# Kernel tuning notes

Measured on AMD Instinct MI355X. Metric: run time of the kernel, lower is better.

Reference implementation:

```python
import jax, jax.numpy as jnp
import numpy as np
import math

B, N, T, D, H, NOUT = 32, 20, 100, 4, 128, 16
E = N * (N - 1)
EPS = 1e-5

def _conv1d(x, w, b):
    # x: [M, Cin, L], w: [Cout, Cin, K] -> [M, Cout, L-K+1] (VALID, stride 1)
    y = jax.lax.conv_general_dilated(x, w, (1,), 'VALID', dimension_numbers=('NCH', 'OIH', 'NCH'))
    return y + b[None, :, None]

def _bn(x, g, b, axes, caxis):
    # training-mode batch norm (biased variance), eps as in torch
    m = jnp.mean(x, axis=axes, keepdims=True)
    v = jnp.var(x, axis=axes, keepdims=True)
    sh = [1] * x.ndim
    sh[caxis] = -1
    return (x - m) / jnp.sqrt(v + EPS) * g.reshape(sh) + b.reshape(sh)

def _mlp(x, w1, b1, w2, b2, g, bb):
    h = jax.nn.elu(x @ w1.T + b1)
    h = jax.nn.elu(h @ w2.T + b2)
    return _bn(h, g, bb, (0, 1), 2)  # BN over B*E samples per feature

def _forward(rel_rec, rel_send, inputs, conv1_w, conv1_b, bn1_g, bn1_b, conv2_w, conv2_b, bn2_g, bn2_b, pred_w, pred_b, att_w, att_b, mlp1_w1, mlp1_b1, mlp1_w2, mlp1_b2, mlp1_g, mlp1_bb, mlp2_w1, mlp2_b1, mlp2_w2, mlp2_b2, mlp2_g, mlp2_bb, mlp3_w1, mlp3_b1, mlp3_w2, mlp3_b2, mlp3_g, mlp3_bb, fc_out_w, fc_out_b):
    Bv, Nv, Tv, Dv = inputs.shape
    Ev = Nv * (Nv - 1)
    # node2edge_temporal: gather sender/receiver trajectories -> [B*E, 2D, T]
    xf = inputs.reshape(Bv, Nv, Tv * Dv)
    recv = jnp.einsum('en,bnf->bef', rel_rec, xf).reshape(Bv * Ev, Tv, Dv).transpose(0, 2, 1)
    send = jnp.einsum('en,bnf->bef', rel_send, xf).reshape(Bv * Ev, Tv, Dv).transpose(0, 2, 1)
    edges = jnp.concatenate([send, recv], axis=1)
    # CNN over time
    h = jax.nn.relu(_conv1d(edges, conv1_w, conv1_b))
    h = _bn(h, bn1_g, bn1_b, (0, 2), 1)
    L = h.shape[-1] // 2
    h = h[:, :, : 2 * L].reshape(h.shape[0], h.shape[1], L, 2).max(axis=-1)  # maxpool k=2 s=2
    h = jax.nn.relu(_conv1d(h, conv2_w, conv2_b))
    h = _bn(h, bn2_g, bn2_b, (0, 2), 1)
    pred = jnp.einsum('bct,oc->bot', h, pred_w[:, :, 0]) + pred_b[None, :, None]
    att = jax.nn.softmax(jnp.einsum('bct,oc->bot', h, att_w[:, :, 0]) + att_b[None, :, None], axis=-1)
    x = (pred * att).mean(axis=-1).reshape(Bv, Ev, -1)  # attention-weighted mean pool
    x = _mlp(x, mlp1_w1, mlp1_b1, mlp1_w2, mlp1_b2, mlp1_g, mlp1_bb)
    x_skip = x
    # edge2node: scatter-mean into receivers (divide by N)
    xn = jnp.einsum('en,beh->bnh', rel_rec, x) / Nv
    xn = _mlp(xn, mlp2_w1, mlp2_b1, mlp2_w2, mlp2_b2, mlp2_g, mlp2_bb)
    # node2edge: gather back to edges
    es = jnp.einsum('en,bnh->beh', rel_send, xn)
    er = jnp.einsum('en,bnh->beh', rel_rec, xn)
    x = jnp.concatenate([es, er, x_skip], axis=2)
    x = _mlp(x, mlp3_w1, mlp3_b1, mlp3_w2, mlp3_b2, mlp3_g, mlp3_bb)
    return x @ fc_out_w.T + fc_out_b

def setup_inputs() -> dict:
    key = jax.random.key(0)
    ks = iter(jax.random.split(key, 64))
    def rn(shape, scale):
        return jax.random.normal(next(ks), shape, dtype=jnp.float32) * scale
    def xav(fo, fi):
        return rn((fo, fi), math.sqrt(2.0 / (fo + fi)))
    inputs = rn((B, N, T, D), 1.0)
    pairs = np.array([(i, j) for i in range(N) for j in range(N) if i != j])
    eye = np.eye(N, dtype=np.float32)
    d = {'inputs': inputs,
         'rel_rec': jnp.asarray(eye[pairs[:, 0]]),
         'rel_send': jnp.asarray(eye[pairs[:, 1]])}
    d['conv1_w'] = rn((H, 2 * D, 5), math.sqrt(2.0 / (5 * H)))
    d['conv1_b'] = jnp.full((H,), 0.1, jnp.float32)
    d['bn1_g'] = jnp.ones((H,), jnp.float32); d['bn1_b'] = jnp.zeros((H,), jnp.float32)
    d['conv2_w'] = rn((H, H, 5), math.sqrt(2.0 / (5 * H)))
    d['conv2_b'] = jnp.full((H,), 0.1, jnp.float32)
    d['bn2_g'] = jnp.ones((H,), jnp.float32); d['bn2_b'] = jnp.zeros((H,), jnp.float32)
    d['pred_w'] = rn((H, H, 1), math.sqrt(2.0 / H))
    d['pred_b'] = jnp.full((H,), 0.1, jnp.float32)
    d['att_w'] = rn((1, H, 1), math.sqrt(2.0))
    d['att_b'] = jnp.full((1,), 0.1, jnp.float32)
    for nm, fi in (('mlp1', H), ('mlp2', H), ('mlp3', 3 * H)):
        d[nm + '_w1'] = xav(H, fi); d[nm + '_b1'] = jnp.full((H,), 0.1, jnp.float32)
        d[nm + '_w2'] = xav(H, H); d[nm + '_b2'] = jnp.full((H,), 0.1, jnp.float32)
        d[nm + '_g'] = jnp.ones((H,), jnp.float32); d[nm + '_bb'] = jnp.zeros((H,), jnp.float32)
    d['fc_out_w'] = xav(NOUT, H)
    d['fc_out_b'] = jnp.full((NOUT,), 0.1, jnp.float32)
    return d

def reference(inputs, rel_rec, rel_send, conv1_w, conv1_b, bn1_g, bn1_b, conv2_w, conv2_b, bn2_g, bn2_b, pred_w, pred_b, att_w, att_b, mlp1_w1, mlp1_b1, mlp1_w2, mlp1_b2, mlp1_g, mlp1_bb, mlp2_w1, mlp2_b1, mlp2_w2, mlp2_b2, mlp2_g, mlp2_bb, mlp3_w1, mlp3_b1, mlp3_w2, mlp3_b2, mlp3_g, mlp3_bb, fc_out_w, fc_out_b):
    return _forward(rel_rec, rel_send, inputs, conv1_w, conv1_b, bn1_g, bn1_b, conv2_w, conv2_b, bn2_g, bn2_b, pred_w, pred_b, att_w, att_b, mlp1_w1, mlp1_b1, mlp1_w2, mlp1_b2, mlp1_g, mlp1_bb, mlp2_w1, mlp2_b1, mlp2_w2, mlp2_b2, mlp2_g, mlp2_bb, mlp3_w1, mlp3_b1, mlp3_w2, mlp3_b2, mlp3_g, mlp3_bb, fc_out_w, fc_out_b)
```

## Files before the change

### kernel.cpp

```cpp
#include <hip/hip_runtime.h>
#include <hip/hip_bf16.h>
#include <hip/hip_fp16.h>

#define BB 32
#define NN 20
#define TT 100
#define DD 4
#define HH 128
#define EE 380
#define BE 12160
#define L1 96
#define LP 48
#define L2 44
#define NOUT 16
#define EPS 1e-5f
#define NREP 64

typedef _Float16 f16x8 __attribute__((ext_vector_type(8)));
typedef _Float16 f16x4 __attribute__((ext_vector_type(4)));
typedef _Float16 f16x2 __attribute__((ext_vector_type(2)));
typedef float f32x4 __attribute__((ext_vector_type(4)));

#define S_BIAS2 0
#define S_BN1_SC 256
#define S_BN2_SC 768

#define OFF_STATS 0ULL
#define OFF_SIDX 16384ULL
#define OFF_RIDX 18432ULL
#define OFF_INC 20480ULL
#define OFF_Y23 24576ULL
#define OFF_X 149446656ULL
#define OFF_BUFA 155672576ULL
#define OFF_BUFB 161898496ULL
#define OFF_XN 168124416ULL
#define OFF_T640 168452096ULL
#define OFF_REPM 168779776ULL
#define OFF_MP 171958272ULL
#define OFF_APACK OFF_T640
#define OFF_APACK1 (OFF_T640 + 163840ULL)
#define OFF_PWT (OFF_T640 + 180224ULL)
#define OFF_W2SUM (OFF_T640 + 245760ULL)
#define OFF_REP1 OFF_BUFA
#define OFF_REP2 (OFF_BUFA + 65536ULL)
#define MP_M1W1 0
#define MP_M1W2 16384
#define MP_M2W1 32768
#define MP_M2W2 49152
#define MP_M3W2 65536
#define MP_M3W1 81920

__device__ __forceinline__ float eluf(float v) { return v > 0.f ? v : expm1f(v); }

__global__ __launch_bounds__(256) void k_prep(const float* __restrict__ rel_rec,
                                              const float* __restrict__ rel_send,
                                              const float* __restrict__ w2,
                                              const float* __restrict__ w1,
                                              const float* __restrict__ pred_w,
                                              const float* __restrict__ m1w1,
                                              const float* __restrict__ m1w2,
                                              const float* __restrict__ m2w1,
                                              const float* __restrict__ m2w2,
                                              const float* __restrict__ m3w1,
                                              const float* __restrict__ m3w2,
                                              _Float16* __restrict__ apack,
                                              _Float16* __restrict__ apack1,
                                              float* __restrict__ pwt,
                                              float* __restrict__ w2sum,
                                              _Float16* __restrict__ mp,
                                              float* rep1, float* rep2, float* repm,
                                              int* sidx, int* ridx, int* inc) {
    int b = blockIdx.x;
    int tid = threadIdx.x;
    int l = tid & 63;
    if (b < 40) {
        int f = b * 4 + (tid >> 6);
        int m0 = f & 7, ks = f >> 3, s = ks & 3, k = ks >> 2;
        int m = m0 * 16 + (l & 15);
        int cbase = 32 * s + (l >> 4) * 8;
#pragma unroll
        for (int j = 0; j < 8; ++j)
            apack[(f * 64 + l) * 8 + j] = (_Float16)w2[m * 640 + (cbase + j) * 5 + k];
    } else if (b < 44) {
        int f = (b - 40) * 4 + (tid >> 6);
        int m0 = f & 7, s = f >> 3;
        int m = m0 * 16 + (l & 15);
        int cbase = 32 * s + (l >> 4) * 8;
#pragma unroll
        for (int j = 0; j < 8; ++j) {
            int c = cbase + j;
            int k = c >> 3, ci = c & 7;
            apack1[(f * 64 + l) * 8 + j] = (k < 5) ? (_Float16)w1[m * 40 + ci * 5 + k]
                                                   : (_Float16)0.f;
        }
    } else if (b == 44) {
        for (int i = tid; i < NREP * 256; i += 256) { rep1[i] = 0.f; rep2[i] = 0.f; }
        for (int i = tid; i < 3 * NREP * 256; i += 256) repm[i] = 0.f;
        for (int e = tid; e < EE; e += 256) {
            int s = 0, r = 0;
            for (int n = 0; n < NN; ++n) {
                if (rel_send[e * NN + n] > 0.5f) s = n;
                if (rel_rec[e * NN + n] > 0.5f) r = n;
            }
            sidx[e] = s; ridx[e] = r;
        }
        __syncthreads();
        if (tid < NN) {
            int k = 0;
            for (int e = 0; e < EE; ++e)
                if (ridx[e] == tid) inc[tid * (NN - 1) + (k++)] = e;
        }
    } else if (b < 53) {
        int idx = (b - 45) * 2048 + tid;
        for (int rep = 0; rep < 8; ++rep, idx += 256) {
            int o = idx >> 7, c = idx & 127;
            pwt[c * 128 + o] = pred_w[idx];
        }
    } else if (b < 117) {
        int idx = b - 53;
        const float* W; _Float16* dst; int K;
        if (idx < 8)       { W = m1w1; dst = mp + MP_M1W1; K = 128; }
        else if (idx < 16) { W = m1w2; dst = mp + MP_M1W2; K = 128; idx -= 8; }
        else if (idx < 24) { W = m2w1; dst = mp + MP_M2W1; K = 128; idx -= 16; }
        else if (idx < 32) { W = m2w2; dst = mp + MP_M2W2; K = 128; idx -= 24; }
        else if (idx < 40) { W = m3w2; dst = mp + MP_M3W2; K = 128; idx -= 32; }
        else               { W = m3w1; dst = mp + MP_M3W1; K = 384; idx -= 40; }
        int f = idx * 4 + (tid >> 6);
        int s = f >> 3, m0 = f & 7;
        int m = m0 * 16 + (l & 15);
        int cb = 32 * s + (l >> 4) * 8;
#pragma unroll
        for (int j = 0; j < 8; ++j)
            dst[(f * 64 + l) * 8 + j] = (_Float16)W[m * K + cb + j];
    } else {
        int idx = (b - 117) * 2048 + tid;
        for (int rep = 0; rep < 8; ++rep, idx += 256) {
            const float* wr = w2 + idx * 5;
            w2sum[idx] = wr[0] + wr[1] + wr[2] + wr[3] + wr[4];
        }
    }
}

__global__ __launch_bounds__(256) void k_conv1_stats(const float* __restrict__ inputs,
                                                     const _Float16* __restrict__ apack1,
                                                     const float* __restrict__ conv1_b,
                                                     const int* __restrict__ sidx,
                                                     const int* __restrict__ ridx,
                                                     float* rep1,
                                                     _Float16* __restrict__ y2p) {
    __shared__ __align__(16) _Float16 s_edgesT[104 * 8];
    __shared__ __align__(16) _Float16 s_y2t[48 * 136];
    int be = blockIdx.x;
    int b = be / EE, e = be - b * EE;
    int sn = sidx[e], rn = ridx[e];
    float* rep = rep1 + (be & (NREP - 1)) * 256;
    for (int i = threadIdx.x; i < 200; i += 256) {
        int side = (i >= 100) ? 1 : 0;
        int t = i - side * 100;
        int n = side ? rn : sn;
        float4 v = *(const float4*)(inputs + ((long long)(b * NN + n) * TT + t) * DD);
        f16x4 o = {(_Float16)v.x, (_Float16)v.y, (_Float16)v.z, (_Float16)v.w};
        *(f16x4*)(&s_edgesT[t * 8 + side * 4]) = o;
    }
    if (threadIdx.x < 32) s_edgesT[800 + threadIdx.x] = (_Float16)0.f;
    __syncthreads();
    int w = threadIdx.x >> 6, lane = threadIdx.x & 63;
    int quad = lane >> 4, l15 = lane & 15;
    f32x4 acc1[2][6];
#pragma unroll
    for (int m = 0; m < 2; ++m)
#pragma unroll
        for (int nt = 0; nt < 6; ++nt) acc1[m][nt] = (f32x4){0.f, 0.f, 0.f, 0.f};
    {
        const f16x8* Ap = (const f16x8*)apack1;
#pragma unroll
        for (int s = 0; s < 2; ++s) {
            f16x8 a0 = Ap[(s * 8 + 2 * w) * 64 + lane];
            f16x8 a1 = Ap[(s * 8 + 2 * w + 1) * 64 + lane];
#pragma unroll
            for (int nt = 0; nt < 6; ++nt) {
                f16x8 bfr = *(const f16x8*)(&s_edgesT[(nt * 16 + l15 + 4 * s + quad) * 8]);
                acc1[0][nt] = __builtin_amdgcn_mfma_f32_16x16x32_f16(a0, bfr, acc1[0][nt], 0, 0, 0);
                acc1[1][nt] = __builtin_amdgcn_mfma_f32_16x16x32_f16(a1, bfr, acc1[1][nt], 0, 0, 0);
            }
        }
    }
#pragma unroll
    for (int m = 0; m < 2; ++m) {
        int co0 = (2 * w + m) * 16 + quad * 4;
        float ss[4] = {0.f, 0.f, 0.f, 0.f}, qq[4] = {0.f, 0.f, 0.f, 0.f};
#pragma unroll
        for (int nt = 0; nt < 6; ++nt) {
            int t = nt * 16 + l15;
#pragma unroll
            for (int r = 0; r < 4; ++r) {
                float v = fmaxf(acc1[m][nt][r] + conv1_b[co0 + r], 0.f);
                ss[r] += v; qq[r] += v * v;
                float p = __shfl_xor(v, 1);
                if ((l15 & 1) == 0)
                    s_y2t[(t >> 1) * 136 + co0 + r] = (_Float16)fmaxf(v, p);
            }
        }
#pragma unroll
        for (int r = 0; r < 4; ++r) {
            float s = ss[r], q = qq[r];
            s += __shfl_xor(s, 1); s += __shfl_xor(s, 2); s += __shfl_xor(s, 4); s += __shfl_xor(s, 8);
            q += __shfl_xor(q, 1); q += __shfl_xor(q, 2); q += __shfl_xor(q, 4); q += __shfl_xor(q, 8);
            if (l15 == 0) {
                atomicAdd(&rep[co0 + r], s);
                atomicAdd(&rep[128 + co0 + r], q);
            }
        }
    }
    __syncthreads();
    _Float16* dst = y2p + (long long)be * 6144;
    for (int chunk = threadIdx.x; chunk < 768; chunk += 256) {
        int row = chunk >> 4, off = (chunk & 15) * 8;
        *(f16x8*)(dst + row * 128 + off) = *(const f16x8*)(&s_y2t[row * 136 + off]);
    }
}

__global__ void k_finalize_rep(float* __restrict__ rep, float* stats, int scIdx,
                               const float* __restrict__ g, const float* __restrict__ bb,
                               float inv_count) {
    int j = threadIdx.x;
    float s = 0.f, q = 0.f;
    for (int i = 0; i < NREP; ++i) {
        s += rep[i * 256 + j];
        q += rep[i * 256 + 128 + j];
    }
    for (int i = 0; i < NREP; ++i) {
        rep[i * 256 + j] = 0.f;
        rep[i * 256 + 128 + j] = 0.f;
    }
    float m = s * inv_count;
    float v = fmaxf(q * inv_count - m * m, 0.f);
    float sc = g[j] * rsqrtf(v + EPS);
    stats[scIdx + j] = sc;
    stats[scIdx + 128 + j] = bb[j] - m * sc;
}

__global__ void k_finalize_bn1(float* __restrict__ rep, float* stats,
                               const float* __restrict__ g, const float* __restrict__ bb,
                               const float* __restrict__ w2sum, const float* __restrict__ conv2_b,
                               float inv_count) {
    __shared__ float s_sh[128];
    int j = threadIdx.x;
    float s = 0.f, q = 0.f;
    for (int i = 0; i < NREP; ++i) {
        s += rep[i * 256 + j];
        q += rep[i * 256 + 128 + j];
    }
    for (int i = 0; i < NREP; ++i) {
        rep[i * 256 + j] = 0.f;
        rep[i * 256 + 128 + j] = 0.f;
    }
    float m = s * inv_count;
    float v = fmaxf(q * inv_count - m * m, 0.f);
    float sc = g[j] * rsqrtf(v + EPS);
    float sh = bb[j] - m * sc;
    stats[S_BN1_SC + j] = sc;
    stats[S_BN1_SC + 128 + j] = sh;
    s_sh[j] = sh;
    __syncthreads();
    float acc = conv2_b[j];
    for (int ci = 0; ci < 128; ++ci)
        acc = fmaf(w2sum[j * 128 + ci], s_sh[ci], acc);
    stats[S_BIAS2 + j] = acc;
}

__global__ __launch_bounds__(256) void k_scale(_Float16* __restrict__ apack,
                                               const float* __restrict__ stats) {
    int tid = threadIdx.x, l = tid & 63;
    int f = blockIdx.x * 4 + (tid >> 6);
    int s = (f >> 3) & 3;
    int cbase = 32 * s + (l >> 4) * 8;
    _Float16* p = apack + (f * 64 + l) * 8;
#pragma unroll
    for (int j = 0; j < 8; ++j)
        p[j] = (_Float16)((float)p[j] * stats[S_BN1_SC + cbase + j]);
}

__global__ __launch_bounds__(512, 6) void k_conv2(_Float16* __restrict__ y23,
                                                  const _Float16* __restrict__ apack,
                                                  const float* __restrict__ stats,
                                                  float* rep2) {
    __shared__ __align__(16) _Float16 s_y2t[2][48 * 136];
    int tid = threadIdx.x;
    long long be0 = (long long)blockIdx.x * 2;
    for (int i = tid; i < 1536; i += 512) {
        int ed = i / 768, rem = i - ed * 768;
        *(f16x8*)(&s_y2t[ed][(rem >> 4) * 136 + (rem & 15) * 8]) =
            *(const f16x8*)(y23 + (be0 + ed) * 6144 + rem * 8);
    }
    __syncthreads();
    int w = tid >> 6, lane = tid & 63;
    int quad = lane >> 4, l15 = lane & 15;
    int g2 = w & 3, ep = w >> 2;
    const char* base = (const char*)&s_y2t[ep][0];
    int rb0 = quad * 16 + l15 * 272;
    f32x4 acc[2][3];
#pragma unroll
    for (int m = 0; m < 2; ++m)
#pragma unroll
        for (int nt = 0; nt < 3; ++nt) acc[m][nt] = (f32x4){0.f, 0.f, 0.f, 0.f};
    const f16x8* Ap = (const f16x8*)apack;
    f16x8 amA[2], amB[2];
#pragma unroll
    for (int m = 0; m < 2; ++m) amA[m] = Ap[(g2 * 2 + m) * 64 + lane];
#define C2_STEP(AM, IT)                                                               \
    do {                                                                              \
        int k = (IT) >> 2, s = (IT) & 3;                                              \
        int rbase = k * 272 + s * 64 + rb0;                                           \
        _Pragma("unroll")                                                             \
        for (int nt = 0; nt < 3; ++nt) {                                              \
            int ro = rbase + nt * (16 * 272);                                         \
            if (nt == 2) { int rr = 32 + l15 + k; if (rr > 47) ro -= (rr - 47) * 272; } \
            f16x8 bfr = *(const f16x8*)(base + ro);                                   \
            acc[0][nt] = __builtin_amdgcn_mfma_f32_16x16x32_f16(AM[0], bfr, acc[0][nt], 0, 0, 0); \
            acc[1][nt] = __builtin_amdgcn_mfma_f32_16x16x32_f16(AM[1], bfr, acc[1][nt], 0, 0, 0); \
        }                                                                             \
    } while (0)
    for (int it = 0; it < 20; it += 2) {
#pragma unroll
        for (int m = 0; m < 2; ++m) amB[m] = Ap[((it + 1) * 8 + g2 * 2 + m) * 64 + lane];
        C2_STEP(amA, it);
        if (it + 2 < 20) {
#pragma unroll
            for (int m = 0; m < 2; ++m) amA[m] = Ap[((it + 2) * 8 + g2 * 2 + m) * 64 + lane];
        }
        C2_STEP(amB, it + 1);
    }
#undef C2_STEP
    long long be = be0 + ep;
    _Float16* y3 = y23 + be * 6144;
    float* rep = rep2 + ((int)(be & (NREP - 1))) * 256;
#pragma unroll
    for (int m = 0; m < 2; ++m) {
        int co0 = (g2 * 2 + m) * 16 + quad * 4;
        float4 bs = *(const float4*)(stats + S_BIAS2 + co0);
        float ssum[4] = {0.f, 0.f, 0.f, 0.f}, qsum[4] = {0.f, 0.f, 0.f, 0.f};
#pragma unroll
        for (int nt = 0; nt < 3; ++nt) {
            int t = nt * 16 + l15;
            if (t < 44) {
                float v0 = fmaxf(acc[m][nt][0] + bs.x, 0.f);
                float v1 = fmaxf(acc[m][nt][1] + bs.y, 0.f);
                float v2 = fmaxf(acc[m][nt][2] + bs.z, 0.f);
                float v3 = fmaxf(acc[m][nt][3] + bs.w, 0.f);
                f16x4 o = {(_Float16)v0, (_Float16)v1, (_Float16)v2, (_Float16)v3};
                *(f16x4*)(y3 + t * 128 + co0) = o;
                ssum[0] += v0; qsum[0] += v0 * v0;
                ssum[1] += v1; qsum[1] += v1 * v1;
                ssum[2] += v2; qsum[2] += v2 * v2;
                ssum[3] += v3; qsum[3] += v3 * v3;
            }
        }
#pragma unroll
        for (int r = 0; r < 4; ++r) {
            float s = ssum[r], q = qsum[r];
            s += __shfl_xor(s, 1); s += __shfl_xor(s, 2); s += __shfl_xor(s, 4); s += __shfl_xor(s, 8);
            q += __shfl_xor(q, 1); q += __shfl_xor(q, 2); q += __shfl_xor(q, 4); q += __shfl_xor(q, 8);
            if (l15 == 0) {
                atomicAdd(&rep[co0 + r], s);
                atomicAdd(&rep[128 + co0 + r], q);
            }
        }
    }
}

__global__ __launch_bounds__(256) void k_predatt(const _Float16* __restrict__ y23,
                                                 const float* __restrict__ stats,
                                                 const float* __restrict__ att_w,
                                                 const float* __restrict__ att_b,
                                                 const float* __restrict__ pwt,
                                                 const float* __restrict__ pred_b,
                                                 float* __restrict__ x) {
    __shared__ float h[44 * 132];
    __shared__ float s_att[48];
    __shared__ float s_p1[256];
    __shared__ float s_p2[256];
    __shared__ float s_sc[128], s_sh[128];
    int be = blockIdx.x, tid = threadIdx.x;
    if (tid < 128) {
        s_sc[tid] = stats[S_BN2_SC + tid];
        s_sh[tid] = stats[S_BN2_SC + 128 + tid];
    }
    __syncthreads();
    const _Float16* yp = y23 + (long long)be * 6144;
    for (int i = tid; i < 704; i += 256) {
        int t = i >> 4, c0 = (i & 15) * 8;
        f16x8 v = *(const f16x8*)(yp + i * 8);
        float4 a, bq;
        a.x = fmaf((float)v[0], s_sc[c0 + 0], s_sh[c0 + 0]);
        a.y = fmaf((float)v[1], s_sc[c0 + 1], s_sh[c0 + 1]);
        a.z = fmaf((float)v[2], s_sc[c0 + 2], s_sh[c0 + 2]);
        a.w = fmaf((float)v[3], s_sc[c0 + 3], s_sh[c0 + 3]);
        bq.x = fmaf((float)v[4], s_sc[c0 + 4], s_sh[c0 + 4]);
        bq.y = fmaf((float)v[5], s_sc[c0 + 5], s_sh[c0 + 5]);
        bq.z = fmaf((float)v[6], s_sc[c0 + 6], s_sh[c0 + 6]);
        bq.w = fmaf((float)v[7], s_sc[c0 + 7], s_sh[c0 + 7]);
        *(float4*)(&h[t * 132 + c0]) = a;
        *(float4*)(&h[t * 132 + c0 + 4]) = bq;
    }
    __syncthreads();
    int w = tid >> 6, lane = tid & 63;
    {
        float aw0 = att_w[lane], aw1 = att_w[64 + lane];
        for (int tt = 0; tt < 11; ++tt) {
            int t = w * 11 + tt;
            float p = h[t * 132 + lane] * aw0 + h[t * 132 + 64 + lane] * aw1;
            p += __shfl_xor(p, 1); p += __shfl_xor(p, 2); p += __shfl_xor(p, 4);
            p += __shfl_xor(p, 8); p += __shfl_xor(p, 16); p += __shfl_xor(p, 32);
            if (lane == 0) s_att[t] = p + att_b[0];
        }
    }
    __syncthreads();
    if (w == 0) {
        float v = (lane < 44) ? s_att[lane] : -1e30f;
        float m = v;
        m = fmaxf(m, __shfl_xor(m, 1)); m = fmaxf(m, __shfl_xor(m, 2));
        m = fmaxf(m, __shfl_xor(m, 4)); m = fmaxf(m, __shfl_xor(m, 8));
        m = fmaxf(m, __shfl_xor(m, 16)); m = fmaxf(m, __shfl_xor(m, 32));
        float ev = (lane < 44) ? expf(v - m) : 0.f;
        float ss = ev;
        ss += __shfl_xor(ss, 1); ss += __shfl_xor(ss, 2); ss += __shfl_xor(ss, 4);
        ss += __shfl_xor(ss, 8); ss += __shfl_xor(ss, 16); ss += __shfl_xor(ss, 32);
        if (lane < 44) s_att[lane] = ev / ss;
    }
    __syncthreads();
    {
        int c = tid & 127, hh = tid >> 7;
        float a = 0.f;
        for (int t = hh * 22; t < hh * 22 + 22; ++t) a = fmaf(h[t * 132 + c], s_att[t], a);
        s_p1[tid] = a;
    }
    __syncthreads();
    {
        int o = tid & 127, hh = tid >> 7;
        float a = 0.f;
        for (int c = hh * 64; c < hh * 64 + 64; ++c) {
            float hw = s_p1[c] + s_p1[128 + c];
            a = fmaf(pwt[c * 128 + o], hw, a);
        }
        s_p2[tid] = a;
    }
    __syncthreads();
    if (tid < 128) {
        float a = s_p2[tid] + s_p2[128 + tid] + pred_b[tid];
        x[(long long)be * 128 + tid] = a * (1.0f / 44.0f);
    }
}

__global__ __launch_bounds__(256) void k_mlp2x(const float* __restrict__ in,
                                               const _Float16* __restrict__ wp1,
                                               const float* __restrict__ b1,
                                               const _Float16* __restrict__ wp2,
                                               const float* __restrict__ b2,
                                               float* __restrict__ out,
                                               float* __restrict__ repm) {
    __shared__ __align__(16) _Float16 s_in[64 * 136];
    __shared__ __align__(16) _Float16 s_mid[64 * 136];
    int tid = threadIdx.x;
    long long r0 = (long long)blockIdx.x * 64;
    {
        const float4* src = (const float4*)(in + r0 * 128);
        for (int i = tid; i < 2048; i += 256) {
            int row = i >> 5, c0 = (i & 31) * 4;
            float4 v = src[i];
            f16x4 o = {(_Float16)v.x, (_Float16)v.y, (_Float16)v.z, (_Float16)v.w};
            *(f16x4*)(&s_in[row * 136 + c0]) = o;
        }
    }
    __syncthreads();
    int w = tid >> 6, lane = tid & 63, quad = lane >> 4, l15 = lane & 15;
    {
        f32x4 acc[2][4];
#pragma unroll
        for (int m = 0; m < 2; ++m)
#pragma unroll
            for (int nt = 0; nt < 4; ++nt) acc[m][nt] = (f32x4){0.f, 0.f, 0.f, 0.f};
        const f16x8* Ap = (const f16x8*)wp1;
#pragma unroll
        for (int s = 0; s < 4; ++s) {
            f16x8 a0 = Ap[(s * 8 + 2 * w) * 64 + lane];
            f16x8 a1 = Ap[(s * 8 + 2 * w + 1) * 64 + lane];
#pragma unroll
            for (int nt = 0; nt < 4; ++nt) {
                f16x8 bfr = *(const f16x8*)((const char*)s_in + (nt * 16 + l15) * 272 + 64 * s + quad * 16);
                acc[0][nt] = __builtin_amdgcn_mfma_f32_16x16x32_f16(a0, bfr, acc[0][nt], 0, 0, 0);
                acc[1][nt] = __builtin_amdgcn_mfma_f32_16x16x32_f16(a1, bfr, acc[1][nt], 0, 0, 0);
            }
        }
#pragma unroll
        for (int m = 0; m < 2; ++m) {
            int j0 = (2 * w + m) * 16 + quad * 4;
            float4 bs = *(const float4*)(b1 + j0);
#pragma unroll
            for (int nt = 0; nt < 4; ++nt) {
                int row = nt * 16 + l15;
                f16x4 o = {(_Float16)eluf(acc[m][nt][0] + bs.x),
                           (_Float16)eluf(acc[m][nt][1] + bs.y),
                           (_Float16)eluf(acc[m][nt][2] + bs.z),
                           (_Float16)eluf(acc[m][nt][3] + bs.w)};
                *(f16x4*)(&s_mid[row * 136 + j0]) = o;
            }
        }
    }
    __syncthreads();
    {
        f32x4 acc[2][4];
#pragma unroll
        for (int m = 0; m < 2; ++m)
#pragma unroll
            for (int nt = 0; nt < 4; ++nt) acc[m][nt] = (f32x4){0.f, 0.f, 0.f, 0.f};
        const f16x8* Ap = (const f16x8*)wp2;
#pragma unroll
        for (int s = 0; s < 4; ++s) {
            f16x8 a0 = Ap[(s * 8 + 2 * w) * 64 + lane];
            f16x8 a1 = Ap[(s * 8 + 2 * w + 1) * 64 + lane];
#pragma unroll
            for (int nt = 0; nt < 4; ++nt) {
                f16x8 bfr = *(const f16x8*)((const char*)s_mid + (nt * 16 + l15) * 272 + 64 * s + quad * 16);
                acc[0][nt] = __builtin_amdgcn_mfma_f32_16x16x32_f16(a0, bfr, acc[0][nt], 0, 0, 0);
                acc[1][nt] = __builtin_amdgcn_mfma_f32_16x16x32_f16(a1, bfr, acc[1][nt], 0, 0, 0);
            }
        }
#pragma unroll
        for (int m = 0; m < 2; ++m) {
            int j0 = (2 * w + m) * 16 + quad * 4;
            float4 bs = *(const float4*)(b2 + j0);
            float ss[4] = {0.f, 0.f, 0.f, 0.f}, qq[4] = {0.f, 0.f, 0.f, 0.f};
#pragma unroll
            for (int nt = 0; nt < 4; ++nt) {
                int row = nt * 16 + l15;
                float v0 = eluf(acc[m][nt][0] + bs.x);
                float v1 = eluf(acc[m][nt][1] + bs.y);
                float v2 = eluf(acc[m][nt][2] + bs.z);
                float v3 = eluf(acc[m][nt][3] + bs.w);
                float4 o = {v0, v1, v2, v3};
                *(float4*)(out + (r0 + row) * 128 + j0) = o;
                ss[0] += v0; qq[0] += v0 * v0;
                ss[1] += v1; qq[1] += v1 * v1;
                ss[2] += v2; qq[2] += v2 * v2;
                ss[3] += v3; qq[3] += v3 * v3;
            }
            float* rep = repm + (blockIdx.x & (NREP - 1)) * 256;
#pragma unroll
            for (int r = 0; r < 4; ++r) {
                float s = ss[r], q = qq[r];
                s += __shfl_xor(s, 1); s += __shfl_xor(s, 2); s += __shfl_xor(s, 4); s += __shfl_xor(s, 8);
                q += __shfl_xor(q, 1); q += __shfl_xor(q, 2); q += __shfl_xor(q, 4); q += __shfl_xor(q, 8);
                if (l15 == 0) {
                    atomicAdd(&rep[j0 + r], s);
                    atomicAdd(&rep[128 + j0 + r], q);
                }
            }
        }
    }
}

__global__ __launch_bounds__(256) void k_mlp3x(const float* __restrict__ xn,
                                               const float* __restrict__ bufB,
                                               const int* __restrict__ sidx,
                                               const int* __restrict__ ridx,
                                               const float* __restrict__ repm1,
                                               const float* __restrict__ repm2,
                                               const float* __restrict__ m1g,
                                               const float* __restrict__ m1bb,
                                               const float* __restrict__ m2g,
                                               const float* __restrict__ m2bb,
                                               const _Float16* __restrict__ wp1,
                                               const float* __restrict__ b1,
                                               const _Float16* __restrict__ wp2,
                                               const float* __restrict__ b2,
                                               float* __restrict__ out,
                                               float* __restrict__ repm3) {
    __shared__ __align__(16) _Float16 s_b[64 * 392];
    __shared__ __align__(16) _Float16 s_mid[64 * 136];
    __shared__ float s_st[4][128];
    __shared__ int s_s[64], s_r[64];
    int tid = threadIdx.x;
    long long r0 = (long long)blockIdx.x * 64;
    if (tid < 128) {
        float s = 0.f, q = 0.f;
        for (int i = 0; i < NREP; ++i) {
            s += repm2[i * 256 + tid];
            q += repm2[i * 256 + 128 + tid];
        }
        float mm = s * (1.0f / (float)(BB * NN));
        float vv = fmaxf(q * (1.0f / (float)(BB * NN)) - mm * mm, 0.f);
        float sc = m2g[tid] * rsqrtf(vv + EPS);
        s_st[0][tid] = sc;
        s_st[1][tid] = m2bb[tid] - mm * sc;
        s = 0.f; q = 0.f;
        for (int i = 0; i < NREP; ++i) {
            s += repm1[i * 256 + tid];
            q += repm1[i * 256 + 128 + tid];
        }
        mm = s * (1.0f / (float)BE);
        vv = fmaxf(q * (1.0f / (float)BE) - mm * mm, 0.f);
        sc = m1g[tid] * rsqrtf(vv + EPS);
        s_st[2][tid] = sc;
        s_st[3][tid] = m1bb[tid] - mm * sc;
    }
    if (tid < 64) {
        int r = (int)r0 + tid, b = r / EE, ed = r - b * EE;
        s_s[tid] = (b * NN + sidx[ed]) * 128;
        s_r[tid] = (b * NN + ridx[ed]) * 128;
    }
    __syncthreads();
    for (int i = tid; i < 8192; i += 256) {
        int row = i >> 7, j = i & 127;
        float sc2 = s_st[0][j], sh2 = s_st[1][j];
        s_b[row * 392 + j] = (_Float16)fmaf(xn[s_s[row] + j], sc2, sh2);
        s_b[row * 392 + 128 + j] = (_Float16)fmaf(xn[s_r[row] + j], sc2, sh2);
        s_b[row * 392 + 256 + j] = (_Float16)fmaf(bufB[(r0 + row) * 128 + j], s_st[2][j], s_st[3][j]);
    }
    __syncthreads();
    int w = tid >> 6, lane = tid & 63, quad = lane >> 4, l15 = lane & 15;
    {
        f32x4 acc[2][4];
#pragma unroll
        for (int m = 0; m < 2; ++m)
#pragma unroll
            for (int nt = 0; nt < 4; ++nt) acc[m][nt] = (f32x4){0.f, 0.f, 0.f, 0.f};
        const f16x8* Ap = (const f16x8*)wp1;
#pragma unroll
        for (int s = 0; s < 12; ++s) {
            f16x8 a0 = Ap[(s * 8 + 2 * w) * 64 + lane];
            f16x8 a1 = Ap[(s * 8 + 2 * w + 1) * 64 + lane];
#pragma unroll
            for (int nt = 0; nt < 4; ++nt) {
                f16x8 bfr = *(const f16x8*)((const char*)s_b + (nt * 16 + l15) * 784 + 64 * s + quad * 16);
                acc[0][nt] = __builtin_amdgcn_mfma_f32_16x16x32_f16(a0, bfr, acc[0][nt], 0, 0, 0);
                acc[1][nt] = __builtin_amdgcn_mfma_f32_16x16x32_f16(a1, bfr, acc[1][nt], 0, 0, 0);
            }
        }
#pragma unroll
        for (int m = 0; m < 2; ++m) {
            int j0 = (2 * w + m) * 16 + quad * 4;
            float4 bs = *(const float4*)(b1 + j0);
#pragma unroll
            for (int nt = 0; nt < 4; ++nt) {
                int row = nt * 16 + l15;
                f16x4 o = {(_Float16)eluf(acc[m][nt][0] + bs.x),
                           (_Float16)eluf(acc[m][nt][1] + bs.y),
                           (_Float16)eluf(acc[m][nt][2] + bs.z),
                           (_Float16)eluf(acc[m][nt][3] + bs.w)};
                *(f16x4*)(&s_mid[row * 136 + j0]) = o;
            }
        }
    }
    __syncthreads();
    {
        f32x4 acc[2][4];
#pragma unroll
        for (int m = 0; m < 2; ++m)
#pragma unroll
            for (int nt = 0; nt < 4; ++nt) acc[m][nt] = (f32x4){0.f, 0.f, 0.f, 0.f};
        const f16x8* Ap = (const f16x8*)wp2;
#pragma unroll
        for (int s = 0; s < 4; ++s) {
            f16x8 a0 = Ap[(s * 8 + 2 * w) * 64 + lane];
            f16x8 a1 = Ap[(s * 8 + 2 * w + 1) * 64 + lane];
#pragma unroll
            for (int nt = 0; nt < 4; ++nt) {
                f16x8 bfr = *(const f16x8*)((const char*)s_mid + (nt * 16 + l15) * 272 + 64 * s + quad * 16);
                acc[0][nt] = __builtin_amdgcn_mfma_f32_16x16x32_f16(a0, bfr, acc[0][nt], 0, 0, 0);
                acc[1][nt] = __builtin_amdgcn_mfma_f32_16x16x32_f16(a1, bfr, acc[1][nt], 0, 0, 0);
            }
        }
#pragma unroll
        for (int m = 0; m < 2; ++m) {
            int j0 = (2 * w + m) * 16 + quad * 4;
            float4 bs = *(const float4*)(b2 + j0);
            float ss[4] = {0.f, 0.f, 0.f, 0.f}, qq[4] = {0.f, 0.f, 0.f, 0.f};
#pragma unroll
            for (int nt = 0; nt < 4; ++nt) {
                int row = nt * 16 + l15;
                float v0 = eluf(acc[m][nt][0] + bs.x);
                float v1 = eluf(acc[m][nt][1] + bs.y);
                float v2 = eluf(acc[m][nt][2] + bs.z);
                float v3 = eluf(acc[m][nt][3] + bs.w);
                float4 o = {v0, v1, v2, v3};
                *(float4*)(out + (r0 + row) * 128 + j0) = o;
                ss[0] += v0; qq[0] += v0 * v0;
                ss[1] += v1; qq[1] += v1 * v1;
                ss[2] += v2; qq[2] += v2 * v2;
                ss[3] += v3; qq[3] += v3 * v3;
            }
            float* rep = repm3 + (blockIdx.x & (NREP - 1)) * 256;
#pragma unroll
            for (int r = 0; r < 4; ++r) {
                float s = ss[r], q = qq[r];
                s += __shfl_xor(s, 1); s += __shfl_xor(s, 2); s += __shfl_xor(s, 4); s += __shfl_xor(s, 8);
                q += __shfl_xor(q, 1); q += __shfl_xor(q, 2); q += __shfl_xor(q, 4); q += __shfl_xor(q, 8);
                if (l15 == 0) {
                    atomicAdd(&rep[j0 + r], s);
                    atomicAdd(&rep[128 + j0 + r], q);
                }
            }
        }
    }
}

__global__ __launch_bounds__(128) void k_e2n(const float* __restrict__ bufB,
                                             const int* __restrict__ inc,
                                             const float* __restrict__ repm1,
                                             const float* __restrict__ m1g,
                                             const float* __restrict__ m1bb,
                                             float* __restrict__ xn) {
    int bn = blockIdx.x;
    int b = bn / NN, n = bn - b * NN;
    int j = threadIdx.x;
    float s0 = 0.f, q0 = 0.f;
    for (int i = 0; i < NREP; ++i) {
        s0 += repm1[i * 256 + j];
        q0 += repm1[i * 256 + 128 + j];
    }
    float mm = s0 * (1.0f / (float)BE);
    float vv = fmaxf(q0 * (1.0f / (float)BE) - mm * mm, 0.f);
    float sc = m1g[j] * rsqrtf(vv + EPS);
    float sh = m1bb[j] - mm * sc;
    float s = 0.f;
    for (int k = 0; k < NN - 1; ++k) {
        int e = inc[n * (NN - 1) + k];
        s += bufB[(long long)(b * EE + e) * 128 + j];
    }
    xn[bn * 128 + j] = (s * sc + (float)(NN - 1) * sh) * (1.0f / (float)NN);
}

__global__ __launch_bounds__(256) void k_fcout(const float* __restrict__ h2,
                                               const float* __restrict__ repm3,
                                               const float* __restrict__ m3g,
                                               const float* __restrict__ m3bb,
                                               const float* __restrict__ fcw,
                                               const float* __restrict__ fcb,
                                               float* __restrict__ out) {
    __shared__ float s_x[16 * 129];
    __shared__ float s_w[16 * 129];
    __shared__ float s_sc[128], s_sh[128];
    int r0 = blockIdx.x * 16;
    int tid = threadIdx.x;
    if (tid < 128) {
        float s = 0.f, q = 0.f;
        for (int i = 0; i < NREP; ++i) {
            s += repm3[i * 256 + tid];
            q += repm3[i * 256 + 128 + tid];
        }
        float mm = s * (1.0f / (float)BE);
        float vv = fmaxf(q * (1.0f / (float)BE) - mm * mm, 0.f);
        float sc = m3g[tid] * rsqrtf(vv + EPS);
        s_sc[tid] = sc;
        s_sh[tid] = m3bb[tid] - mm * sc;
    }
    __syncthreads();
    for (int i = tid; i < 16 * 128; i += 256) {
        int rr = i >> 7, j = i & 127;
        s_x[rr * 129 + j] = fmaf(h2[(long long)(r0 + rr) * 128 + j], s_sc[j], s_sh[j]);
    }
    for (int i = tid; i < 16 * 128; i += 256) {
        int o = i >> 7, j = i & 127;
        s_w[o * 129 + j] = fcw[i];
    }
    __syncthreads();
    int rl = tid >> 4, o = tid & 15;
    float a = fcb[o];
    for (int j = 0; j < 128; ++j) a = fmaf(s_x[rl * 129 + j], s_w[o * 129 + j], a);
    out[(long long)(r0 + rl) * 16 + o] = a;
}

extern "C" void kernel_launch(void* const* d_in, const int* in_sizes, int n_in,
                              void* d_out, int out_size, void* d_ws, size_t ws_size,
                              hipStream_t stream) {
    const float* inputs = (const float*)d_in[0];
    const float* rel_rec = (const float*)d_in[1];
    const float* rel_send = (const float*)d_in[2];
    const float* conv1_w = (const float*)d_in[3];
    const float* conv1_b = (const float*)d_in[4];
    const float* bn1_g = (const float*)d_in[5];
    const float* bn1_b = (const float*)d_in[6];
    const float* conv2_w = (const float*)d_in[7];
    const float* conv2_b = (const float*)d_in[8];
    const float* bn2_g = (const float*)d_in[9];
    const float* bn2_b = (const float*)d_in[10];
    const float* pred_w = (const float*)d_in[11];
    const float* pred_b = (const float*)d_in[12];
    const float* att_w = (const float*)d_in[13];
    const float* att_b = (const float*)d_in[14];
    const float* m1w1 = (const float*)d_in[15];
    const float* m1b1 = (const float*)d_in[16];
    const float* m1w2 = (const float*)d_in[17];
    const float* m1b2 = (const float*)d_in[18];
    const float* m1g = (const float*)d_in[19];
    const float* m1bb = (const float*)d_in[20];
    const float* m2w1 = (const float*)d_in[21];
    const float* m2b1 = (const float*)d_in[22];
    const float* m2w2 = (const float*)d_in[23];
    const float* m2b2 = (const float*)d_in[24];
    const float* m2g = (const float*)d_in[25];
    const float* m2bb = (const float*)d_in[26];
    const float* m3w1 = (const float*)d_in[27];
    const float* m3b1 = (const float*)d_in[28];
    const float* m3w2 = (const float*)d_in[29];
    const float* m3b2 = (const float*)d_in[30];
    const float* m3g = (const float*)d_in[31];
    const float* m3bb = (const float*)d_in[32];
    const float* fcw = (const float*)d_in[33];
    const float* fcb = (const float*)d_in[34];

    char* ws = (char*)d_ws;
    float* stats = (float*)(ws + OFF_STATS);
    int* sidx = (int*)(ws + OFF_SIDX);
    int* ridx = (int*)(ws + OFF_RIDX);
    int* inc = (int*)(ws + OFF_INC);
    _Float16* y23 = (_Float16*)(ws + OFF_Y23);
    float* x = (float*)(ws + OFF_X);
    float* bufB = (float*)(ws + OFF_BUFB);
    float* xn = (float*)(ws + OFF_XN);
    _Float16* apack = (_Float16*)(ws + OFF_APACK);
    _Float16* apack1 = (_Float16*)(ws + OFF_APACK1);
    float* pwt = (float*)(ws + OFF_PWT);
    float* w2sum = (float*)(ws + OFF_W2SUM);
    float* rep1 = (float*)(ws + OFF_REP1);
    float* rep2 = (float*)(ws + OFF_REP2);
    float* repm1 = (float*)(ws + OFF_REPM);
    float* repm2 = (float*)(ws + OFF_REPM + 65536ULL);
    float* repm3 = (float*)(ws + OFF_REPM + 131072ULL);
    _Float16* mp = (_Float16*)(ws + OFF_MP);
    float* outp = (float*)d_out;

    hipLaunchKernelGGL(k_prep, dim3(125), dim3(256), 0, stream,
                       rel_rec, rel_send, conv2_w, conv1_w, pred_w,
                       m1w1, m1w2, m2w1, m2w2, m3w1, m3w2,
                       apack, apack1, pwt, w2sum, mp, rep1, rep2, repm1, sidx, ridx, inc);
    hipLaunchKernelGGL(k_conv1_stats, dim3(BE), dim3(256), 0, stream,
                       inputs, apack1, conv1_b, sidx, ridx, rep1, y23);
    hipLaunchKernelGGL(k_finalize_bn1, dim3(1), dim3(128), 0, stream,
                       rep1, stats, bn1_g, bn1_b, w2sum, conv2_b, 1.0f / (float)(BE * L1));
    hipLaunchKernelGGL(k_scale, dim3(40), dim3(256), 0, stream, apack, stats);
    hipLaunchKernelGGL(k_conv2, dim3(BE / 2), dim3(512), 0, stream,
                       y23, apack, stats, rep2);
    hipLaunchKernelGGL(k_finalize_rep, dim3(1), dim3(128), 0, stream,
                       rep2, stats, S_BN2_SC, bn2_g, bn2_b, 1.0f / (float)(BE * L2));
    hipLaunchKernelGGL(k_predatt, dim3(BE), dim3(256), 0, stream,
                       y23, stats, att_w, att_b, pwt, pred_b, x);
    hipLaunchKernelGGL(k_mlp2x, dim3(BE / 64), dim3(256), 0, stream,
                       x, mp + MP_M1W1, m1b1, mp + MP_M1W2, m1b2, bufB, repm1);
    hipLaunchKernelGGL(k_e2n, dim3(BB * NN), dim3(128), 0, stream, bufB, inc, repm1, m1g, m1bb, xn);
    hipLaunchKernelGGL(k_mlp2x, dim3(BB * NN / 64), dim3(256), 0, stream,
                       xn, mp + MP_M2W1, m2b1, mp + MP_M2W2, m2b2, xn, repm2);
    hipLaunchKernelGGL(k_mlp3x, dim3(BE / 64), dim3(256), 0, stream,
                       xn, bufB, sidx, ridx, repm1, repm2, m1g, m1bb, m2g, m2bb,
                       mp + MP_M3W1, m3b1, mp + MP_M3W2, m3b2, bufB, repm3);
    hipLaunchKernelGGL(k_fcout, dim3(BE / 16), dim3(256), 0, stream,
                       bufB, repm3, m3g, m3bb, fcw, fcb, outp);
    (void)in_sizes; (void)n_in; (void)out_size; (void)ws_size;
}
```

Measured before the change: 594.7 us.

## Make conv2 blocks persistent over four edge-pair tiles with double-buffered LDS prefetch

Each k_conv2 block now loops over four consecutive edge-pair tiles instead of one, and the grid shrinks by a factor of four. While the MFMA loop runs on the current tile, the next tile's activations are prefetched into registers and then written to the other half of a double-buffered LDS array. This hides global load latency behind compute and amortises block launch and setup. In exchange, LDS per block doubles, which can lower the number of resident blocks per CU. The smaller grid also gives fewer blocks to spread across the device.

```diff
diff --git a/kernel.cpp b/kernel.cpp
--- a/kernel.cpp
+++ b/kernel.cpp
@@ -285,29 +285,46 @@
                                                   const _Float16* __restrict__ apack,
                                                   const float* __restrict__ stats,
                                                   float* rep2) {
-    __shared__ __align__(16) _Float16 s_y2t[2][48 * 136];
+    __shared__ __align__(16) _Float16 s_y2t[2][2][48 * 136];
     int tid = threadIdx.x;
-    long long be0 = (long long)blockIdx.x * 2;
-    for (int i = tid; i < 1536; i += 512) {
-        int ed = i / 768, rem = i - ed * 768;
-        *(f16x8*)(&s_y2t[ed][(rem >> 4) * 136 + (rem & 15) * 8]) =
-            *(const f16x8*)(y23 + (be0 + ed) * 6144 + rem * 8);
-    }
-    __syncthreads();
     int w = tid >> 6, lane = tid & 63;
     int quad = lane >> 4, l15 = lane & 15;
     int g2 = w & 3, ep = w >> 2;
-    const char* base = (const char*)&s_y2t[ep][0];
     int rb0 = quad * 16 + l15 * 272;
-    f32x4 acc[2][3];
-#pragma unroll
-    for (int m = 0; m < 2; ++m)
-#pragma unroll
-        for (int nt = 0; nt < 3; ++nt) acc[m][nt] = (f32x4){0.f, 0.f, 0.f, 0.f};
     const f16x8* Ap = (const f16x8*)apack;
-    f16x8 amA[2], amB[2];
-#pragma unroll
-    for (int m = 0; m < 2; ++m) amA[m] = Ap[(g2 * 2 + m) * 64 + lane];
+    int sed[3], srem[3];
+#pragma unroll
+    for (int j = 0; j < 3; ++j) {
+        int i = tid + 512 * j;
+        sed[j] = (i >= 768) ? 1 : 0;
+        srem[j] = i - sed[j] * 768;
+    }
+    long long tile0 = (long long)blockIdx.x * 4;
+    f16x8 st[3];
+#pragma unroll
+    for (int j = 0; j < 3; ++j)
+        st[j] = *(const f16x8*)(y23 + (tile0 * 2 + sed[j]) * 6144 + srem[j] * 8);
+    int cur = 0;
+    for (int tt = 0; tt < 4; ++tt) {
+        long long e2 = (tile0 + tt) * 2;
+#pragma unroll
+        for (int j = 0; j < 3; ++j)
+            *(f16x8*)(&s_y2t[cur][sed[j]][(srem[j] >> 4) * 136 + (srem[j] & 15) * 8]) = st[j];
+        __syncthreads();
+        if (tt < 3) {
+#pragma unroll
+            for (int j = 0; j < 3; ++j)
+                st[j] = *(const f16x8*)(y23 + (e2 + 2 + sed[j]) * 6144 + srem[j] * 8);
+        }
+        const char* base = (const char*)&s_y2t[cur][ep][0];
+        f32x4 acc[2][3];
+#pragma unroll
+        for (int m = 0; m < 2; ++m)
+#pragma unroll
+            for (int nt = 0; nt < 3; ++nt) acc[m][nt] = (f32x4){0.f, 0.f, 0.f, 0.f};
+        f16x8 amA[2], amB[2];
+#pragma unroll
+        for (int m = 0; m < 2; ++m) amA[m] = Ap[(g2 * 2 + m) * 64 + lane];
 #define C2_STEP(AM, IT)                                                               \
     do {                                                                              \
         int k = (IT) >> 2, s = (IT) & 3;                                              \
@@ -321,51 +338,53 @@
             acc[1][nt] = __builtin_amdgcn_mfma_f32_16x16x32_f16(AM[1], bfr, acc[1][nt], 0, 0, 0); \
         }                                                                             \
     } while (0)
-    for (int it = 0; it < 20; it += 2) {
-#pragma unroll
-        for (int m = 0; m < 2; ++m) amB[m] = Ap[((it + 1) * 8 + g2 * 2 + m) * 64 + lane];
-        C2_STEP(amA, it);
-        if (it + 2 < 20) {
-#pragma unroll
-            for (int m = 0; m < 2; ++m) amA[m] = Ap[((it + 2) * 8 + g2 * 2 + m) * 64 + lane];
-        }
-        C2_STEP(amB, it + 1);
-    }
+        for (int it = 0; it < 20; it += 2) {
+#pragma unroll
+            for (int m = 0; m < 2; ++m) amB[m] = Ap[((it + 1) * 8 + g2 * 2 + m) * 64 + lane];
+            C2_STEP(amA, it);
+            if (it + 2 < 20) {
+#pragma unroll
+                for (int m = 0; m < 2; ++m) amA[m] = Ap[((it + 2) * 8 + g2 * 2 + m) * 64 + lane];
+            }
+            C2_STEP(amB, it + 1);
+        }
 #undef C2_STEP
-    long long be = be0 + ep;
-    _Float16* y3 = y23 + be * 6144;
-    float* rep = rep2 + ((int)(be & (NREP - 1))) * 256;
-#pragma unroll
-    for (int m = 0; m < 2; ++m) {
-        int co0 = (g2 * 2 + m) * 16 + quad * 4;
-        float4 bs = *(const float4*)(stats + S_BIAS2 + co0);
-        float ssum[4] = {0.f, 0.f, 0.f, 0.f}, qsum[4] = {0.f, 0.f, 0.f, 0.f};
-#pragma unroll
-        for (int nt = 0; nt < 3; ++nt) {
-            int t = nt * 16 + l15;
-            if (t < 44) {
-                float v0 = fmaxf(acc[m][nt][0] + bs.x, 0.f);
-                float v1 = fmaxf(acc[m][nt][1] + bs.y, 0.f);
-                float v2 = fmaxf(acc[m][nt][2] + bs.z, 0.f);
-                float v3 = fmaxf(acc[m][nt][3] + bs.w, 0.f);
-                f16x4 o = {(_Float16)v0, (_Float16)v1, (_Float16)v2, (_Float16)v3};
-                *(f16x4*)(y3 + t * 128 + co0) = o;
-                ssum[0] += v0; qsum[0] += v0 * v0;
-                ssum[1] += v1; qsum[1] += v1 * v1;
-                ssum[2] += v2; qsum[2] += v2 * v2;
-                ssum[3] += v3; qsum[3] += v3 * v3;
-            }
-        }
-#pragma unroll
-        for (int r = 0; r < 4; ++r) {
-            float s = ssum[r], q = qsum[r];
-            s += __shfl_xor(s, 1); s += __shfl_xor(s, 2); s += __shfl_xor(s, 4); s += __shfl_xor(s, 8);
-            q += __shfl_xor(q, 1); q += __shfl_xor(q, 2); q += __shfl_xor(q, 4); q += __shfl_xor(q, 8);
-            if (l15 == 0) {
-                atomicAdd(&rep[co0 + r], s);
-                atomicAdd(&rep[128 + co0 + r], q);
-            }
-        }
+        long long be = e2 + ep;
+        _Float16* y3 = y23 + be * 6144;
+        float* rep = rep2 + ((int)(be & (NREP - 1))) * 256;
+#pragma unroll
+        for (int m = 0; m < 2; ++m) {
+            int co0 = (g2 * 2 + m) * 16 + quad * 4;
+            float4 bs = *(const float4*)(stats + S_BIAS2 + co0);
+            float ssum[4] = {0.f, 0.f, 0.f, 0.f}, qsum[4] = {0.f, 0.f, 0.f, 0.f};
+#pragma unroll
+            for (int nt = 0; nt < 3; ++nt) {
+                int t = nt * 16 + l15;
+                if (t < 44) {
+                    float v0 = fmaxf(acc[m][nt][0] + bs.x, 0.f);
+                    float v1 = fmaxf(acc[m][nt][1] + bs.y, 0.f);
+                    float v2 = fmaxf(acc[m][nt][2] + bs.z, 0.f);
+                    float v3 = fmaxf(acc[m][nt][3] + bs.w, 0.f);
+                    f16x4 o = {(_Float16)v0, (_Float16)v1, (_Float16)v2, (_Float16)v3};
+                    *(f16x4*)(y3 + t * 128 + co0) = o;
+                    ssum[0] += v0; qsum[0] += v0 * v0;
+                    ssum[1] += v1; qsum[1] += v1 * v1;
+                    ssum[2] += v2; qsum[2] += v2 * v2;
+                    ssum[3] += v3; qsum[3] += v3 * v3;
+                }
+            }
+#pragma unroll
+            for (int r = 0; r < 4; ++r) {
+                float s = ssum[r], q = qsum[r];
+                s += __shfl_xor(s, 1); s += __shfl_xor(s, 2); s += __shfl_xor(s, 4); s += __shfl_xor(s, 8);
+                q += __shfl_xor(q, 1); q += __shfl_xor(q, 2); q += __shfl_xor(q, 4); q += __shfl_xor(q, 8);
+                if (l15 == 0) {
+                    atomicAdd(&rep[co0 + r], s);
+                    atomicAdd(&rep[128 + co0 + r], q);
+                }
+            }
+        }
+        cur ^= 1;
     }
 }
 
@@ -840,7 +859,7 @@
     hipLaunchKernelGGL(k_finalize_bn1, dim3(1), dim3(128), 0, stream,
                        rep1, stats, bn1_g, bn1_b, w2sum, conv2_b, 1.0f / (float)(BE * L1));
     hipLaunchKernelGGL(k_scale, dim3(40), dim3(256), 0, stream, apack, stats);
-    hipLaunchKernelGGL(k_conv2, dim3(BE / 2), dim3(512), 0, stream,
+    hipLaunchKernelGGL(k_conv2, dim3(BE / 8), dim3(512), 0, stream,
                        y23, apack, stats, rep2);
     hipLaunchKernelGGL(k_finalize_rep, dim3(1), dim3(128), 0, stream,
                        rep2, stats, S_BN2_SC, bn2_g, bn2_b, 1.0f / (float)(BE * L2));
```

Result: slower. 1.111 ms (+86.7%).

## Recompute conv1 inside conv2 instead of storing pooled activations

Applied to the files above, without the earlier changes.

The conv1 stats kernel now only accumulates BN1 statistics and no longer writes the pooled conv1 output to global memory. The conv2 kernel gathers the raw edge inputs itself, recomputes conv1 with MFMA, applies ReLU and maxpool into shared memory, and then runs conv2 as before. This removes a large global write and read of intermediate activations (BE*6144 fp16 each way) at the cost of doing the conv1 MFMAs twice. Occupancy for conv2 is lowered in launch bounds and shared memory grows.

```diff
diff --git a/kernel.cpp b/kernel.cpp
--- a/kernel.cpp
+++ b/kernel.cpp
@@ -146,10 +146,8 @@
                                                      const float* __restrict__ conv1_b,
                                                      const int* __restrict__ sidx,
                                                      const int* __restrict__ ridx,
-                                                     float* rep1,
-                                                     _Float16* __restrict__ y2p) {
+                                                     float* rep1) {
     __shared__ __align__(16) _Float16 s_edgesT[104 * 8];
-    __shared__ __align__(16) _Float16 s_y2t[48 * 136];
     int be = blockIdx.x;
     int b = be / EE, e = be - b * EE;
     int sn = sidx[e], rn = ridx[e];
@@ -191,14 +189,10 @@
         float ss[4] = {0.f, 0.f, 0.f, 0.f}, qq[4] = {0.f, 0.f, 0.f, 0.f};
 #pragma unroll
         for (int nt = 0; nt < 6; ++nt) {
-            int t = nt * 16 + l15;
 #pragma unroll
             for (int r = 0; r < 4; ++r) {
                 float v = fmaxf(acc1[m][nt][r] + conv1_b[co0 + r], 0.f);
                 ss[r] += v; qq[r] += v * v;
-                float p = __shfl_xor(v, 1);
-                if ((l15 & 1) == 0)
-                    s_y2t[(t >> 1) * 136 + co0 + r] = (_Float16)fmaxf(v, p);
             }
         }
 #pragma unroll
@@ -211,12 +205,6 @@
                 atomicAdd(&rep[128 + co0 + r], q);
             }
         }
-    }
-    __syncthreads();
-    _Float16* dst = y2p + (long long)be * 6144;
-    for (int chunk = threadIdx.x; chunk < 768; chunk += 256) {
-        int row = chunk >> 4, off = (chunk & 15) * 8;
-        *(f16x8*)(dst + row * 128 + off) = *(const f16x8*)(&s_y2t[row * 136 + off]);
     }
 }
 
@@ -281,23 +269,73 @@
         p[j] = (_Float16)((float)p[j] * stats[S_BN1_SC + cbase + j]);
 }
 
-__global__ __launch_bounds__(512, 6) void k_conv2(_Float16* __restrict__ y23,
+__global__ __launch_bounds__(512, 4) void k_conv2(const float* __restrict__ inputs,
+                                                  const int* __restrict__ sidx,
+                                                  const int* __restrict__ ridx,
+                                                  const _Float16* __restrict__ apack1,
+                                                  const float* __restrict__ conv1_b,
+                                                  _Float16* __restrict__ y23,
                                                   const _Float16* __restrict__ apack,
                                                   const float* __restrict__ stats,
                                                   float* rep2) {
+    __shared__ __align__(16) _Float16 s_edgesT[2][104 * 8];
     __shared__ __align__(16) _Float16 s_y2t[2][48 * 136];
     int tid = threadIdx.x;
     long long be0 = (long long)blockIdx.x * 2;
-    for (int i = tid; i < 1536; i += 512) {
-        int ed = i / 768, rem = i - ed * 768;
-        *(f16x8*)(&s_y2t[ed][(rem >> 4) * 136 + (rem & 15) * 8]) =
-            *(const f16x8*)(y23 + (be0 + ed) * 6144 + rem * 8);
-    }
+    for (int i = tid; i < 400; i += 512) {
+        int ed = i / 200, rem = i - ed * 200;
+        int side = (rem >= 100) ? 1 : 0;
+        int t = rem - side * 100;
+        int be = (int)be0 + ed;
+        int b = be / EE, e = be - b * EE;
+        int n = side ? ridx[e] : sidx[e];
+        float4 v = *(const float4*)(inputs + ((long long)(b * NN + n) * TT + t) * DD);
+        f16x4 o = {(_Float16)v.x, (_Float16)v.y, (_Float16)v.z, (_Float16)v.w};
+        *(f16x4*)(&s_edgesT[ed][t * 8 + side * 4]) = o;
+    }
+    if (tid < 64) s_edgesT[tid >> 5][800 + (tid & 31)] = (_Float16)0.f;
     __syncthreads();
     int w = tid >> 6, lane = tid & 63;
     int quad = lane >> 4, l15 = lane & 15;
-    int g2 = w & 3, ep = w >> 2;
-    const char* base = (const char*)&s_y2t[ep][0];
+    int w4 = w & 3, ep = w >> 2;
+    {
+        f32x4 acc1[2][6];
+#pragma unroll
+        for (int m = 0; m < 2; ++m)
+#pragma unroll
+            for (int nt = 0; nt < 6; ++nt) acc1[m][nt] = (f32x4){0.f, 0.f, 0.f, 0.f};
+        const f16x8* Ap1 = (const f16x8*)apack1;
+#pragma unroll
+        for (int s = 0; s < 2; ++s) {
+            f16x8 a0 = Ap1[(s * 8 + 2 * w4) * 64 + lane];
+            f16x8 a1 = Ap1[(s * 8 + 2 * w4 + 1) * 64 + lane];
+#pragma unroll
+            for (int nt = 0; nt < 6; ++nt) {
+                f16x8 bfr = *(const f16x8*)(&s_edgesT[ep][(nt * 16 + l15 + 4 * s + quad) * 8]);
+                acc1[0][nt] = __builtin_amdgcn_mfma_f32_16x16x32_f16(a0, bfr, acc1[0][nt], 0, 0, 0);
+                acc1[1][nt] = __builtin_amdgcn_mfma_f32_16x16x32_f16(a1, bfr, acc1[1][nt], 0, 0, 0);
+            }
+        }
+#pragma unroll
+        for (int m = 0; m < 2; ++m) {
+            int co0 = (2 * w4 + m) * 16 + quad * 4;
+#pragma unroll
+            for (int nt = 0; nt < 6; ++nt) {
+                int t = nt * 16 + l15;
+#pragma unroll
+                for (int r = 0; r < 4; ++r) {
+                    float v = fmaxf(acc1[m][nt][r] + conv1_b[co0 + r], 0.f);
+                    float p = __shfl_xor(v, 1);
+                    if ((l15 & 1) == 0)
+                        s_y2t[ep][(t >> 1) * 136 + co0 + r] = (_Float16)fmaxf(v, p);
+                }
+            }
+        }
+    }
+    __syncthreads();
+    int g2 = w & 3;
+    int ep2 = w >> 2;
+    const char* base = (const char*)&s_y2t[ep2][0];
     int rb0 = quad * 16 + l15 * 272;
     f32x4 acc[2][3];
 #pragma unroll
@@ -332,7 +370,7 @@
         C2_STEP(amB, it + 1);
     }
 #undef C2_STEP
-    long long be = be0 + ep;
+    long long be = be0 + ep2;
     _Float16* y3 = y23 + be * 6144;
     float* rep = rep2 + ((int)(be & (NREP - 1))) * 256;
 #pragma unroll
@@ -836,12 +874,12 @@
                        m1w1, m1w2, m2w1, m2w2, m3w1, m3w2,
                        apack, apack1, pwt, w2sum, mp, rep1, rep2, repm1, sidx, ridx, inc);
     hipLaunchKernelGGL(k_conv1_stats, dim3(BE), dim3(256), 0, stream,
-                       inputs, apack1, conv1_b, sidx, ridx, rep1, y23);
+                       inputs, apack1, conv1_b, sidx, ridx, rep1);
     hipLaunchKernelGGL(k_finalize_bn1, dim3(1), dim3(128), 0, stream,
                        rep1, stats, bn1_g, bn1_b, w2sum, conv2_b, 1.0f / (float)(BE * L1));
     hipLaunchKernelGGL(k_scale, dim3(40), dim3(256), 0, stream, apack, stats);
     hipLaunchKernelGGL(k_conv2, dim3(BE / 2), dim3(512), 0, stream,
-                       y23, apack, stats, rep2);
+                       inputs, sidx, ridx, apack1, conv1_b, y23, apack, stats, rep2);
     hipLaunchKernelGGL(k_finalize_rep, dim3(1), dim3(128), 0, stream,
                        rep2, stats, S_BN2_SC, bn2_g, bn2_b, 1.0f / (float)(BE * L2));
     hipLaunchKernelGGL(k_predatt, dim3(BE), dim3(256), 0, stream,
```

New measurement: 567.1 us. -4.6%, faster.
